# Optimization experiments

Hardware: AMD Instinct MI355X
Metric: run time of the kernel (lower is better)

## Reference

```python
import jax, jax.numpy as jnp
import numpy as np

L, D, H, F, E, K = 2, 512, 8, 2048, 8, 2
V, B, S, T, PAD = 32000, 2, 1024, 1024, 0


def _pe(n, d):
    pos = jnp.arange(n, dtype=jnp.float32)[:, None]
    div = jnp.exp(jnp.arange(0, d, 2, dtype=jnp.float32) * (-np.log(10000.0) / d))
    pe = jnp.zeros((n, d), jnp.float32)
    pe = pe.at[:, 0::2].set(jnp.sin(pos * div)).at[:, 1::2].set(jnp.cos(pos * div))
    return pe


def _ln(x, g, b):
    m = x.mean(-1, keepdims=True)
    v = ((x - m) ** 2).mean(-1, keepdims=True)
    return (x - m) / jnp.sqrt(v + 1e-5) * g + b


def _mha(q_in, k_in, v_in, w, b, mask):
    # w: [4,D,D] (q,k,v,out), b: [4,D]; mask broadcastable to [B,H,Sq,Sk] (True=keep)
    Bq, Sq, Dm = q_in.shape
    Sk = k_in.shape[1]
    dk = Dm // H
    q = (q_in @ w[0] + b[0]).reshape(Bq, Sq, H, dk).transpose(0, 2, 1, 3)
    k = (k_in @ w[1] + b[1]).reshape(Bq, Sk, H, dk).transpose(0, 2, 1, 3)
    v = (v_in @ w[2] + b[2]).reshape(Bq, Sk, H, dk).transpose(0, 2, 1, 3)
    s = jnp.einsum('bhqd,bhkd->bhqk', q, k) / np.sqrt(dk).astype(np.float32)
    s = jnp.where(mask, s, jnp.float32(-1e9))
    a = jax.nn.softmax(s, axis=-1)
    c = jnp.einsum('bhqk,bhkd->bhqd', a, v).transpose(0, 2, 1, 3).reshape(Bq, Sq, Dm)
    return c @ w[3] + b[3]


def _moe(x, gw, gb, w1, b1, w2, b2):
    # token-choice top-k routing with softmax gate probs (no renormalization)
    Bx, Sx, Dm = x.shape
    N = Bx * Sx
    xf = x.reshape(N, Dm)
    probs = jax.nn.softmax(xf @ gw + gb, axis=-1)              # [N,E]
    topv, topi = jax.lax.top_k(probs, K)                        # [N,K]
    comb = jnp.zeros_like(probs).at[jnp.arange(N)[:, None], topi].set(topv)  # [N,E] sparse combine weights
    h = jax.nn.relu(jnp.einsum('nd,edf->nef', xf, w1) + b1)     # [N,E,F]
    eo = jnp.einsum('nef,efd->ned', h, w2) + b2                 # [N,E,D]
    y = jnp.einsum('ne,ned->nd', comb, eo)
    return y.reshape(Bx, Sx, Dm)


def setup_inputs():
    key = jax.random.key(0)
    ks = iter(jax.random.split(key, 32))
    sd, sf = 1.0 / np.sqrt(D), 1.0 / np.sqrt(F)

    def nrm(shape, scale):
        return jax.random.normal(next(ks), shape, jnp.float32) * np.float32(scale)

    inp = {}
    inp['src'] = jax.random.randint(next(ks), (B, S), 0, V)
    inp['tgt'] = jax.random.randint(next(ks), (B, T), 0, V)
    inp['enc_emb'] = nrm((V, D), 0.02).at[PAD].set(0.0)
    inp['dec_emb'] = nrm((V, D), 0.02).at[PAD].set(0.0)
    inp['enc_attn_w'] = nrm((L, 4, D, D), sd)
    inp['enc_attn_b'] = jnp.zeros((L, 4, D), jnp.float32)
    inp['enc_ln_g'] = jnp.ones((L, 2, D), jnp.float32)
    inp['enc_ln_b'] = jnp.zeros((L, 2, D), jnp.float32)
    inp['enc_gate_w'] = nrm((L, D, E), sd)
    inp['enc_gate_b'] = jnp.zeros((L, E), jnp.float32)
    inp['enc_w1'] = nrm((L, E, D, F), sd)
    inp['enc_b1'] = jnp.zeros((L, E, F), jnp.float32)
    inp['enc_w2'] = nrm((L, E, F, D), sf)
    inp['enc_b2'] = jnp.zeros((L, E, D), jnp.float32)
    inp['dec_sa_w'] = nrm((L, 4, D, D), sd)
    inp['dec_sa_b'] = jnp.zeros((L, 4, D), jnp.float32)
    inp['dec_ca_w'] = nrm((L, 4, D, D), sd)
    inp['dec_ca_b'] = jnp.zeros((L, 4, D), jnp.float32)
    inp['dec_ln_g'] = jnp.ones((L, 3, D), jnp.float32)
    inp['dec_ln_b'] = jnp.zeros((L, 3, D), jnp.float32)
    inp['dec_gate_w'] = nrm((L, D, E), sd)
    inp['dec_gate_b'] = jnp.zeros((L, E), jnp.float32)
    inp['dec_w1'] = nrm((L, E, D, F), sd)
    inp['dec_b1'] = jnp.zeros((L, E, F), jnp.float32)
    inp['dec_w2'] = nrm((L, E, F, D), sf)
    inp['dec_b2'] = jnp.zeros((L, E, D), jnp.float32)
    inp['out_w'] = nrm((D, V), sd)
    inp['out_b'] = jnp.zeros((V,), jnp.float32)
    return inp


def reference(src, tgt, enc_emb, dec_emb, enc_attn_w, enc_attn_b, enc_ln_g, enc_ln_b,
              enc_gate_w, enc_gate_b, enc_w1, enc_b1, enc_w2, enc_b2,
              dec_sa_w, dec_sa_b, dec_ca_w, dec_ca_b, dec_ln_g, dec_ln_b,
              dec_gate_w, dec_gate_b, dec_w1, dec_b1, dec_w2, dec_b2, out_w, out_b):
    src_mask = (src != PAD)[:, None, None, :]                                  # [B,1,1,S]
    causal = jnp.tril(jnp.ones((T, T), bool))
    tgt_mask = (tgt != PAD)[:, None, None, :] & causal[None, None]             # [B,1,T,T]

    x = enc_emb[src] + _pe(S, D)[None]                                         # dropout = identity (eval)
    for l in range(L):
        a = _mha(x, x, x, enc_attn_w[l], enc_attn_b[l], src_mask)
        x = _ln(x + a, enc_ln_g[l, 0], enc_ln_b[l, 0])
        f = _moe(x, enc_gate_w[l], enc_gate_b[l], enc_w1[l], enc_b1[l], enc_w2[l], enc_b2[l])
        x = _ln(x + f, enc_ln_g[l, 1], enc_ln_b[l, 1])
    enc_out = x

    y = dec_emb[tgt] + _pe(T, D)[None]
    for l in range(L):
        a = _mha(y, y, y, dec_sa_w[l], dec_sa_b[l], tgt_mask)
        y = _ln(y + a, dec_ln_g[l, 0], dec_ln_b[l, 0])
        c = _mha(y, enc_out, enc_out, dec_ca_w[l], dec_ca_b[l], src_mask)
        y = _ln(y + c, dec_ln_g[l, 1], dec_ln_b[l, 1])
        f = _moe(y, dec_gate_w[l], dec_gate_b[l], dec_w1[l], dec_b1[l], dec_w2[l], dec_b2[l])
        y = _ln(y + f, dec_ln_g[l, 2], dec_ln_b[l, 2])

    return y @ out_w + out_b                                                    # [B,T,V]
```

## Files before the change

### kernel.cpp

```cpp
#include <hip/hip_runtime.h>
#include <hip/hip_bf16.h>

#define L_ 2
#define D_ 512
#define H_ 8
#define DK_ 64
#define F_ 2048
#define E_ 8
#define V_ 32000
#define B_ 2
#define S_ 1024
#define T_ 1024
#define NTOK (B_*S_)
#define MAXPAD 4608
#define RB64   72
#define QLD 1536

typedef unsigned short u16;
typedef _Float16 f16x8 __attribute__((ext_vector_type(8)));
typedef _Float16 f16x4 __attribute__((ext_vector_type(4)));
typedef float f32x4 __attribute__((ext_vector_type(4)));

__device__ __forceinline__ void gload16(const void* g, const void* l) {
    __builtin_amdgcn_global_load_lds(
        (const __attribute__((address_space(1))) void*)g,
        (__attribute__((address_space(3))) void*)l, 16, 0, 0);
}

__device__ __forceinline__ void split_f16(float v, _Float16& h, _Float16& l) {
    h = (_Float16)v;
    l = (_Float16)(v - (float)h);
}

__global__ __launch_bounds__(256) void embed_pe(const int* __restrict__ toks,
                                                const float* __restrict__ emb,
                                                _Float16* __restrict__ oh,
                                                _Float16* __restrict__ ol, int Slen)
{
    int n = blockIdx.x;
    int spos = n % Slen;
    int tok = toks[n];
    const float* erow = emb + (size_t)tok * D_;
    size_t rb = (size_t)n * D_;
    for (int j = threadIdx.x; j < D_; j += 256) {
        int i = j >> 1;
        float arg = (float)spos * expf(-(float)i * 0.035977892f);
        float pe = (j & 1) ? cosf(arg) : sinf(arg);
        float v = erow[j] + pe;
        _Float16 h, l; split_f16(v, h, l);
        oh[rb + j] = h; ol[rb + j] = l;
    }
}

template<bool WLO>
__global__ __launch_bounds__(256) void transpose_w(const float* __restrict__ in,
                                                   _Float16* __restrict__ oh,
                                                   _Float16* __restrict__ ol, int R, int C)
{
    __shared__ float t[64][65];
    size_t sb = (size_t)blockIdx.z * R * C;
    in += sb; oh += sb; if (WLO) ol += sb;
    int c0 = blockIdx.x * 64, r0 = blockIdx.y * 64;
    int tid = threadIdx.x;
    {
        int r = tid >> 4;
        int cq = (tid & 15) * 4;
        #pragma unroll
        for (int p = 0; p < 4; ++p) {
            int rr = r + p * 16;
            float4 v = *(const float4*)&in[(size_t)(r0 + rr) * C + c0 + cq];
            t[rr][cq] = v.x; t[rr][cq + 1] = v.y; t[rr][cq + 2] = v.z; t[rr][cq + 3] = v.w;
        }
    }
    __syncthreads();
    int rp = (tid & 15) * 4;
    int cb = tid >> 4;
    #pragma unroll
    for (int p = 0; p < 4; ++p) {
        int c = cb + p * 16;
        f16x4 hv, lv;
        #pragma unroll
        for (int j = 0; j < 4; ++j) {
            float v = t[rp + j][c];
            _Float16 h = (_Float16)v;
            hv[j] = h;
            if (WLO) lv[j] = (_Float16)(v - (float)h);
        }
        *(f16x4*)&oh[(size_t)(c0 + c) * R + r0 + rp] = hv;
        if (WLO) *(f16x4*)&ol[(size_t)(c0 + c) * R + r0 + rp] = lv;
    }
}

__global__ __launch_bounds__(256) void transpose_w3(
    const float* __restrict__ i0, _Float16* __restrict__ h0, _Float16* __restrict__ l0,
    const float* __restrict__ i1, _Float16* __restrict__ h1, _Float16* __restrict__ l1,
    const float* __restrict__ i2, _Float16* __restrict__ h2, _Float16* __restrict__ l2)
{
    __shared__ float t[64][65];
    int set = blockIdx.z >> 3, sub = blockIdx.z & 7;
    const float* in = (set == 0) ? i0 : (set == 1) ? i1 : i2;
    _Float16* oh = (set == 0) ? h0 : (set == 1) ? h1 : h2;
    _Float16* ol = (set == 0) ? l0 : (set == 1) ? l1 : l2;
    size_t sb = (size_t)sub * D_ * D_;
    in += sb; oh += sb; ol += sb;
    int c0 = blockIdx.x * 64, r0 = blockIdx.y * 64;
    int tid = threadIdx.x;
    {
        int r = tid >> 4;
        int cq = (tid & 15) * 4;
        #pragma unroll
        for (int p = 0; p < 4; ++p) {
            int rr = r + p * 16;
            float4 v = *(const float4*)&in[(size_t)(r0 + rr) * D_ + c0 + cq];
            t[rr][cq] = v.x; t[rr][cq + 1] = v.y; t[rr][cq + 2] = v.z; t[rr][cq + 3] = v.w;
        }
    }
    __syncthreads();
    int rp = (tid & 15) * 4;
    int cb = tid >> 4;
    #pragma unroll
    for (int p = 0; p < 4; ++p) {
        int c = cb + p * 16;
        f16x4 hv, lv;
        #pragma unroll
        for (int j = 0; j < 4; ++j) {
            float v = t[rp + j][c];
            _Float16 h = (_Float16)v;
            hv[j] = h;
            lv[j] = (_Float16)(v - (float)h);
        }
        *(f16x4*)&oh[(size_t)(c0 + c) * D_ + r0 + rp] = hv;
        *(f16x4*)&ol[(size_t)(c0 + c) * D_ + r0 + rp] = lv;
    }
}

template<int MODE, bool RELU, int OUTMODE, int PASSES, int TM, int TN>
__global__ __launch_bounds__(256, 2) void gemm_mfma(
    const _Float16* __restrict__ Ah, const _Float16* __restrict__ Al,
    const _Float16* __restrict__ Wh, const _Float16* __restrict__ Wl,
    const float* __restrict__ biasbase,
    float* __restrict__ Cf, _Float16* __restrict__ Ch, _Float16* __restrict__ Cl,
    _Float16* __restrict__ vt_h, _Float16* __restrict__ vt_l, int cbase,
    int M, int Kd, int N, int ldc,
    const int* __restrict__ route_tok, const int* __restrict__ rb_expert,
    const int* __restrict__ pad_base, const int* __restrict__ counts)
{
    constexpr int AR = TM / 32;
    constexpr int BR = TN / 32;
    int row0 = blockIdx.x * TM;
    const _Float16* Wmh = Wh;
    const _Float16* Wml = Wl;
    const float* bias = biasbase;
    int vend = M;
    if (MODE != 0) {
        int total = pad_base[E_];
        if (row0 >= total) return;
        int e = rb_expert[row0 >> 6];
        vend = pad_base[e] + counts[e];
        Wmh = Wh + (size_t)e * Kd * N;
        if (PASSES == 3) Wml = Wl + (size_t)e * Kd * N;
        bias = biasbase + (size_t)e * N;
    }
    int col0 = blockIdx.y * TN;
    int tid = threadIdx.x;
    int lane = tid & 63, w = tid >> 6;
    int wm = w >> 1, wn = w & 1;

    __shared__ _Float16 lds[(PASSES == 3 ? 2 : 1) * (TM + TN) * 64];
    _Float16* lAh = lds;
    _Float16* lBh = lds + TM * 64;
    _Float16* lAl = (PASSES == 3) ? lds + (TM + TN) * 64 : nullptr;
    _Float16* lBl = (PASSES == 3) ? lds + (TM + TN) * 64 + TM * 64 : nullptr;

    int srow8 = lane >> 3;
    int q8 = lane & 7;
    size_t aoff[AR], boff[BR];
    #pragma unroll
    for (int j = 0; j < AR; ++j) {
        int m = w * (TM / 4) + j * 8 + srow8;
        int gr = row0 + m;
        int ar = (MODE == 1) ? route_tok[gr] : gr;
        int ss = (q8 ^ (m & 7)) << 3;
        aoff[j] = (size_t)ar * Kd + ss;
    }
    #pragma unroll
    for (int j = 0; j < BR; ++j) {
        int m = w * (TN / 4) + j * 8 + srow8;
        int ss = (q8 ^ (m & 7)) << 3;
        boff[j] = (size_t)(col0 + m) * Kd + ss;
    }

    f32x4 zero4 = {0.f, 0.f, 0.f, 0.f};
    f32x4 acc[AR][BR];
    #pragma unroll
    for (int i = 0; i < AR; ++i)
        #pragma unroll
        for (int j = 0; j < BR; ++j) acc[i][j] = zero4;

    int lm = lane & 15, kg = lane >> 4;

    for (int k0 = 0; k0 < Kd; k0 += 64) {
        #pragma unroll
        for (int j = 0; j < AR; ++j) {
            int lb = (w * (TM / 4) + j * 8) * 64;
            gload16(Ah + aoff[j] + k0, lAh + lb);
            if (PASSES == 3) gload16(Al + aoff[j] + k0, lAl + lb);
        }
        #pragma unroll
        for (int j = 0; j < BR; ++j) {
            int lb = (w * (TN / 4) + j * 8) * 64;
            gload16(Wmh + boff[j] + k0, lBh + lb);
            if (PASSES == 3) gload16(Wml + boff[j] + k0, lBl + lb);
        }
        __syncthreads();
        #pragma unroll
        for (int ks = 0; ks < 2; ++ks) {
            f16x8 ah[AR], bh[BR];
            #pragma unroll
            for (int i = 0; i < AR; ++i) {
                int m = wm * (TM / 2) + i * 16 + lm;
                ah[i] = *(const f16x8*)&lAh[m * 64 + ((((ks << 2) + kg) ^ (m & 7)) << 3)];
            }
            #pragma unroll
            for (int j = 0; j < BR; ++j) {
                int n = wn * (TN / 2) + j * 16 + lm;
                bh[j] = *(const f16x8*)&lBh[n * 64 + ((((ks << 2) + kg) ^ (n & 7)) << 3)];
            }
            #pragma unroll
            for (int i = 0; i < AR; ++i)
                #pragma unroll
                for (int jn = 0; jn < BR; ++jn)
                    acc[i][jn] = __builtin_amdgcn_mfma_f32_16x16x32_f16(ah[i], bh[jn], acc[i][jn], 0, 0, 0);
            if (PASSES == 3) {
                f16x8 bl[BR];
                #pragma unroll
                for (int j = 0; j < BR; ++j) {
                    int n = wn * (TN / 2) + j * 16 + lm;
                    bl[j] = *(const f16x8*)&lBl[n * 64 + ((((ks << 2) + kg) ^ (n & 7)) << 3)];
                }
                #pragma unroll
                for (int i = 0; i < AR; ++i)
                    #pragma unroll
                    for (int jn = 0; jn < BR; ++jn)
                        acc[i][jn] = __builtin_amdgcn_mfma_f32_16x16x32_f16(ah[i], bl[jn], acc[i][jn], 0, 0, 0);
                f16x8 al[AR];
                #pragma unroll
                for (int i = 0; i < AR; ++i) {
                    int m = wm * (TM / 2) + i * 16 + lm;
                    al[i] = *(const f16x8*)&lAl[m * 64 + ((((ks << 2) + kg) ^ (m & 7)) << 3)];
                }
                #pragma unroll
                for (int i = 0; i < AR; ++i)
                    #pragma unroll
                    for (int jn = 0; jn < BR; ++jn)
                        acc[i][jn] = __builtin_amdgcn_mfma_f32_16x16x32_f16(al[i], bh[jn], acc[i][jn], 0, 0, 0);
            }
        }
        __syncthreads();
    }

    float bv[BR];
    #pragma unroll
    for (int jn = 0; jn < BR; ++jn) bv[jn] = bias[col0 + wn * (TN / 2) + jn * 16 + lm];
    int rowb = row0 + wm * (TM / 2) + (lane >> 4) * 4;

    if (OUTMODE == 2 && (col0 + cbase) >= 1024) {
        #pragma unroll
        for (int i = 0; i < AR; ++i) {
            int row = rowb + i * 16;
            int b = row >> 10, q = row & 1023;
            #pragma unroll
            for (int jn = 0; jn < BR; ++jn) {
                int vcol = col0 + cbase - 1024 + wn * (TN / 2) + jn * 16 + lm;
                int hh = vcol >> 6, dd = vcol & 63;
                f16x4 hv, lv;
                #pragma unroll
                for (int r = 0; r < 4; ++r) {
                    float v = acc[i][jn][r] + bv[jn];
                    _Float16 x1, x2; split_f16(v, x1, x2);
                    hv[r] = x1; lv[r] = x2;
                }
                size_t vtoff = ((size_t)((b << 3) + hh) * 64 + dd) * 1024 + q;
                *(f16x4*)&vt_h[vtoff] = hv;
                *(f16x4*)&vt_l[vtoff] = lv;
            }
        }
        return;
    }

    #pragma unroll
    for (int i = 0; i < AR; ++i) {
        #pragma unroll
        for (int r = 0; r < 4; ++r) {
            int row = rowb + i * 16 + r;
            if (MODE != 0 && row >= vend) continue;
            #pragma unroll
            for (int jn = 0; jn < BR; ++jn) {
                float v = acc[i][jn][r] + bv[jn];
                if (RELU) v = fmaxf(v, 0.f);
                int c = col0 + wn * (TN / 2) + jn * 16 + lm;
                if (OUTMODE == 0) {
                    Cf[(size_t)row * ldc + c] = v;
                } else {
                    _Float16 h, l; split_f16(v, h, l);
                    Ch[(size_t)row * ldc + cbase + c] = h;
                    Cl[(size_t)row * ldc + cbase + c] = l;
                }
            }
        }
    }
}

template<int CAUSAL>
__global__ __launch_bounds__(512, 1) void attn_flash(
    const _Float16* __restrict__ qkvh, const _Float16* __restrict__ qkvl,
    const _Float16* __restrict__ vth, const _Float16* __restrict__ vtl,
    const int* __restrict__ ktoks,
    _Float16* __restrict__ ch, _Float16* __restrict__ cl)
{
    int q0 = blockIdx.x * 64;
    int bh = blockIdx.y, b = bh >> 3, h = bh & 7;
    int tid = threadIdx.x, lane = tid & 63, w = tid >> 6;
    int qg = w & 3, kh = w >> 2;
    int lm = lane & 15, kg = lane >> 4;
    int srow8 = lane >> 3, q8 = lane & 7;
    int tb = b * S_;

    __shared__ _Float16 smem[49152];
    _Float16* hb  = smem + kh * 16384;
    _Float16* lKh = hb;
    _Float16* lKl = hb + 4096;
    _Float16* lVh = hb + 8192;
    _Float16* lVl = hb + 12288;
    _Float16* lPh = smem + 32768 + w * 1024;
    _Float16* lPl = smem + 40960 + w * 1024;

    size_t qbase = (size_t)b * S_ * QLD + h * DK_;
    const _Float16* Qh = qkvh + qbase;
    const _Float16* Ql = qkvl + qbase;
    const _Float16* Kh = qkvh + qbase + 512;
    const _Float16* Kl = qkvl + qbase + 512;
    const _Float16* Vh = vth + (size_t)bh * 64 * 1024;
    const _Float16* Vl = vtl + (size_t)bh * 64 * 1024;

    f16x8 qfh[2], qfl[2];
    {
        int qr = q0 + qg * 16 + lm;
        #pragma unroll
        for (int ks = 0; ks < 2; ++ks) {
            qfh[ks] = *(const f16x8*)&Qh[(size_t)qr * QLD + ks * 32 + kg * 8];
            qfl[ks] = *(const f16x8*)&Ql[(size_t)qr * QLD + ks * 32 + kg * 8];
        }
    }

    float mreg[4], lreg[4];
    f32x4 od[4];
    f32x4 zero4 = {0.f, 0.f, 0.f, 0.f};
    #pragma unroll
    for (int r = 0; r < 4; ++r) { mreg[r] = -1e30f; lreg[r] = 0.f; }
    #pragma unroll
    for (int jn = 0; jn < 4; ++jn) od[jn] = zero4;

    int qrow[4];
    #pragma unroll
    for (int r = 0; r < 4; ++r) qrow[r] = q0 + qg * 16 + (lane >> 4) * 4 + r;

    int nkt = CAUSAL ? (q0 >> 6) + 1 : 16;
    int nhalf = (nkt + 1) >> 1;

    for (int it = 0; it < nhalf; ++it) {
        int kt = 2 * it + kh;
        bool active = kt < nkt;
        int k0 = kt * 64;

        if (active) {
            #pragma unroll
            for (int j = 0; j < 2; ++j) {
                int row = qg * 16 + j * 8 + srow8;
                int lb = (qg * 16 + j * 8) * 64;
                int ss = (q8 ^ (row & 7)) << 3;
                gload16(Kh + (size_t)(k0 + row) * QLD + ss, lKh + lb);
                gload16(Kl + (size_t)(k0 + row) * QLD + ss, lKl + lb);
                gload16(Vh + (size_t)row * 1024 + k0 + ss, lVh + lb);
                gload16(Vl + (size_t)row * 1024 + k0 + ss, lVl + lb);
            }
        }
        __syncthreads();

        if (active) {
            bool diag = CAUSAL && (kt == (q0 >> 6));
            f32x4 accs[4];
            #pragma unroll
            for (int jn = 0; jn < 4; ++jn) accs[jn] = zero4;
            #pragma unroll
            for (int ks = 0; ks < 2; ++ks) {
                #pragma unroll
                for (int jn = 0; jn < 4; ++jn) {
                    int n = jn * 16 + lm;
                    int koff = n * 64 + ((((ks << 2) + kg) ^ (n & 7)) << 3);
                    f16x8 bhv = *(const f16x8*)&lKh[koff];
                    f16x8 blv = *(const f16x8*)&lKl[koff];
                    accs[jn] = __builtin_amdgcn_mfma_f32_16x16x32_f16(qfh[ks], bhv, accs[jn], 0, 0, 0);
                    accs[jn] = __builtin_amdgcn_mfma_f32_16x16x32_f16(qfh[ks], blv, accs[jn], 0, 0, 0);
                    accs[jn] = __builtin_amdgcn_mfma_f32_16x16x32_f16(qfl[ks], bhv, accs[jn], 0, 0, 0);
                }
            }

            float sv[4][4];
            #pragma unroll
            for (int jn = 0; jn < 4; ++jn) {
                int kglob = k0 + jn * 16 + lm;
                bool pad_ok = (ktoks[tb + kglob] != 0);
                #pragma unroll
                for (int r = 0; r < 4; ++r) {
                    float s = accs[jn][r] * 0.125f;
                    bool keep = pad_ok && (!diag || kglob <= qrow[r]);
                    sv[jn][r] = keep ? s : -1e9f;
                }
            }
            float pv[4][4];
            #pragma unroll
            for (int r = 0; r < 4; ++r) {
                float tm = fmaxf(fmaxf(sv[0][r], sv[1][r]), fmaxf(sv[2][r], sv[3][r]));
                tm = fmaxf(tm, __shfl_xor(tm, 1));
                tm = fmaxf(tm, __shfl_xor(tm, 2));
                tm = fmaxf(tm, __shfl_xor(tm, 4));
                tm = fmaxf(tm, __shfl_xor(tm, 8));
                float mnew = fmaxf(mreg[r], tm);
                float corr = expf(mreg[r] - mnew);
                lreg[r] *= corr;
                #pragma unroll
                for (int jn = 0; jn < 4; ++jn) od[jn][r] *= corr;
                float psum = 0.f;
                #pragma unroll
                for (int jn = 0; jn < 4; ++jn) {
                    float p = expf(sv[jn][r] - mnew);
                    pv[jn][r] = p;
                    psum += p;
                }
                psum += __shfl_xor(psum, 1);
                psum += __shfl_xor(psum, 2);
                psum += __shfl_xor(psum, 4);
                psum += __shfl_xor(psum, 8);
                lreg[r] += psum;
                mreg[r] = mnew;
            }

            #pragma unroll
            for (int jn = 0; jn < 4; ++jn) {
                int col = jn * 16 + lm;
                #pragma unroll
                for (int r = 0; r < 4; ++r) {
                    int rr = (lane >> 4) * 4 + r;
                    int idx = rr * 64 + (((col >> 3) ^ (rr & 7)) << 3) + (col & 7);
                    _Float16 hh, ll; split_f16(pv[jn][r], hh, ll);
                    lPh[idx] = hh; lPl[idx] = ll;
                }
            }

            #pragma unroll
            for (int ks = 0; ks < 2; ++ks) {
                int poff = lm * 64 + ((((ks << 2) + kg) ^ (lm & 7)) << 3);
                f16x8 pah = *(const f16x8*)&lPh[poff];
                f16x8 pal = *(const f16x8*)&lPl[poff];
                #pragma unroll
                for (int jn = 0; jn < 4; ++jn) {
                    int n = jn * 16 + lm;
                    int noff = n * 64 + ((((ks << 2) + kg) ^ (n & 7)) << 3);
                    f16x8 vbh = *(const f16x8*)&lVh[noff];
                    f16x8 vbl = *(const f16x8*)&lVl[noff];
                    od[jn] = __builtin_amdgcn_mfma_f32_16x16x32_f16(pah, vbh, od[jn], 0, 0, 0);
                    od[jn] = __builtin_amdgcn_mfma_f32_16x16x32_f16(pah, vbl, od[jn], 0, 0, 0);
                    od[jn] = __builtin_amdgcn_mfma_f32_16x16x32_f16(pal, vbh, od[jn], 0, 0, 0);
                }
            }
        }
        __syncthreads();
    }

    float* mrg = (float*)(smem + 32768);
    if (kh == 1) {
        float* mp = mrg + ((size_t)qg * 64 + lane) * 24;
        #pragma unroll
        for (int jn = 0; jn < 4; ++jn)
            #pragma unroll
            for (int r = 0; r < 4; ++r) mp[jn * 4 + r] = od[jn][r];
        #pragma unroll
        for (int r = 0; r < 4; ++r) { mp[16 + r] = mreg[r]; mp[20 + r] = lreg[r]; }
    }
    __syncthreads();
    if (kh == 0) {
        float* mp = mrg + ((size_t)qg * 64 + lane) * 24;
        #pragma unroll
        for (int r = 0; r < 4; ++r) {
            float m1 = mp[16 + r], l1 = mp[20 + r];
            float m = fmaxf(mreg[r], m1);
            float c0 = expf(mreg[r] - m), c1 = expf(m1 - m);
            float inv = 1.0f / (lreg[r] * c0 + l1 * c1);
            size_t rbase = (size_t)(tb + qrow[r]) * D_ + h * DK_;
            #pragma unroll
            for (int jn = 0; jn < 4; ++jn) {
                float o = (od[jn][r] * c0 + mp[jn * 4 + r] * c1) * inv;
                _Float16 hh, ll; split_f16(o, hh, ll);
                int d = jn * 16 + lm;
                ch[rbase + d] = hh; cl[rbase + d] = ll;
            }
        }
    }
}

template<bool GATE>
__global__ __launch_bounds__(256) void ln_add(const _Float16* __restrict__ xh,
                                              const _Float16* __restrict__ xl,
                                              const float* __restrict__ r,
                                              const float* __restrict__ g,
                                              const float* __restrict__ be,
                                              _Float16* __restrict__ oh,
                                              _Float16* __restrict__ ol,
                                              const float* __restrict__ gw,
                                              const float* __restrict__ gbias,
                                              float* __restrict__ lg)
{
    int w = threadIdx.x >> 6, lane = threadIdx.x & 63;
    int row = blockIdx.x * 4 + w;
    int col = lane * 8;
    size_t rb = (size_t)row * D_ + col;
    f16x8 vh = *(const f16x8*)&xh[rb];
    f16x8 vl = *(const f16x8*)&xl[rb];
    float4 ra = *(const float4*)&r[rb];
    float4 rc = *(const float4*)&r[rb + 4];
    float v[8];
    v[0] = (float)vh[0] + (float)vl[0] + ra.x;
    v[1] = (float)vh[1] + (float)vl[1] + ra.y;
    v[2] = (float)vh[2] + (float)vl[2] + ra.z;
    v[3] = (float)vh[3] + (float)vl[3] + ra.w;
    v[4] = (float)vh[4] + (float)vl[4] + rc.x;
    v[5] = (float)vh[5] + (float)vl[5] + rc.y;
    v[6] = (float)vh[6] + (float)vl[6] + rc.z;
    v[7] = (float)vh[7] + (float)vl[7] + rc.w;
    float s = 0.f;
    #pragma unroll
    for (int i = 0; i < 8; ++i) s += v[i];
    #pragma unroll
    for (int off = 32; off; off >>= 1) s += __shfl_xor(s, off);
    float m = s * (1.0f / 512.0f);
    float d[8];
    float q = 0.f;
    #pragma unroll
    for (int i = 0; i < 8; ++i) { d[i] = v[i] - m; q += d[i] * d[i]; }
    #pragma unroll
    for (int off = 32; off; off >>= 1) q += __shfl_xor(q, off);
    float rstd = rsqrtf(q * (1.0f / 512.0f) + 1e-5f);
    float4 ga = *(const float4*)&g[col];
    float4 gc = *(const float4*)&g[col + 4];
    float4 ba = *(const float4*)&be[col];
    float4 bc = *(const float4*)&be[col + 4];
    float gg[8] = {ga.x, ga.y, ga.z, ga.w, gc.x, gc.y, gc.z, gc.w};
    float bb[8] = {ba.x, ba.y, ba.z, ba.w, bc.x, bc.y, bc.z, bc.w};
    float y[8];
    f16x8 ohv, olv;
    #pragma unroll
    for (int i = 0; i < 8; ++i) {
        y[i] = d[i] * rstd * gg[i] + bb[i];
        _Float16 h2, l2; split_f16(y[i], h2, l2);
        ohv[i] = h2; olv[i] = l2;
    }
    *(f16x8*)&oh[rb] = ohv;
    *(f16x8*)&ol[rb] = olv;
    if (GATE) {
        float acc[E_] = {0.f, 0.f, 0.f, 0.f, 0.f, 0.f, 0.f, 0.f};
        #pragma unroll
        for (int i = 0; i < 8; ++i) {
            const float* gp = gw + (size_t)(col + i) * E_;
            float4 g0 = *(const float4*)gp;
            float4 g1 = *(const float4*)(gp + 4);
            acc[0] += y[i] * g0.x; acc[1] += y[i] * g0.y;
            acc[2] += y[i] * g0.z; acc[3] += y[i] * g0.w;
            acc[4] += y[i] * g1.x; acc[5] += y[i] * g1.y;
            acc[6] += y[i] * g1.z; acc[7] += y[i] * g1.w;
        }
        #pragma unroll
        for (int e = 0; e < E_; ++e)
            #pragma unroll
            for (int off = 32; off; off >>= 1) acc[e] += __shfl_xor(acc[e], off);
        if (lane == 0) {
            float* lp = lg + (size_t)row * E_;
            #pragma unroll
            for (int e = 0; e < E_; ++e) lp[e] = acc[e] + gbias[e];
        }
    }
}

__global__ __launch_bounds__(256) void ln_add_moe(const _Float16* __restrict__ xh,
                                                  const _Float16* __restrict__ xl,
                                                  const float* __restrict__ eo,
                                                  const float* __restrict__ topv,
                                                  const int* __restrict__ route_row,
                                                  const float* __restrict__ g,
                                                  const float* __restrict__ be,
                                                  _Float16* __restrict__ oh,
                                                  _Float16* __restrict__ ol)
{
    int w = threadIdx.x >> 6, lane = threadIdx.x & 63;
    int row = blockIdx.x * 4 + w;
    int r0 = route_row[row * 2], r1 = route_row[row * 2 + 1];
    float w0 = topv[row * 2], w1 = topv[row * 2 + 1];
    int col = lane * 8;
    size_t rb = (size_t)row * D_ + col;
    f16x8 vh = *(const f16x8*)&xh[rb];
    f16x8 vl = *(const f16x8*)&xl[rb];
    const float* e0 = eo + (size_t)r0 * D_ + col;
    const float* e1 = eo + (size_t)r1 * D_ + col;
    float4 e0a = *(const float4*)e0;
    float4 e0b = *(const float4*)(e0 + 4);
    float4 e1a = *(const float4*)e1;
    float4 e1b = *(const float4*)(e1 + 4);
    float v[8];
    v[0] = (float)vh[0] + (float)vl[0] + w0 * e0a.x + w1 * e1a.x;
    v[1] = (float)vh[1] + (float)vl[1] + w0 * e0a.y + w1 * e1a.y;
    v[2] = (float)vh[2] + (float)vl[2] + w0 * e0a.z + w1 * e1a.z;
    v[3] = (float)vh[3] + (float)vl[3] + w0 * e0a.w + w1 * e1a.w;
    v[4] = (float)vh[4] + (float)vl[4] + w0 * e0b.x + w1 * e1b.x;
    v[5] = (float)vh[5] + (float)vl[5] + w0 * e0b.y + w1 * e1b.y;
    v[6] = (float)vh[6] + (float)vl[6] + w0 * e0b.z + w1 * e1b.z;
    v[7] = (float)vh[7] + (float)vl[7] + w0 * e0b.w + w1 * e1b.w;
    float s = 0.f;
    #pragma unroll
    for (int i = 0; i < 8; ++i) s += v[i];
    #pragma unroll
    for (int off = 32; off; off >>= 1) s += __shfl_xor(s, off);
    float m = s * (1.0f / 512.0f);
    float d[8];
    float q = 0.f;
// ... 85 lines not shown
        for (int sg = 0; sg < 16; ++sg) {
            int v = segb[t][sg];
            segb[t][sg] = (unsigned short)run;
            run += v;
        }
        cnt[t] = run;
        counts[t] = run;
    }
    __syncthreads();
    if (t < 128) {
        int e = t >> 4, seg = t & 15;
        int run = segb[e][seg];
        #pragma unroll
        for (int i = 0; i < 16; ++i) {
            int c = seg * 16 + i;
            int v = chist[c][e];
            chist[c][e] = (unsigned short)run;
            run += v;
        }
    }
    __syncthreads();

    if (t == 0) {
        int pad = 0;
        for (int e = 0; e < 8; ++e) {
            pb[e] = pad;
            pad_base[e] = pad;
            int nb = (cnt[e] + 63) >> 6;
            for (int rb = 0; rb < nb; ++rb) rb_expert[(pad >> 6) + rb] = e;
            pad += nb << 6;
        }
        pb[8] = pad;
        pad_base[8] = pad;
    }
    __syncthreads();

    if (t < 256) {
        int r[16];
        #pragma unroll
        for (int i = 0; i < 16; ++i) r[i] = eid[t * 16 + i];
        #pragma unroll
        for (int e = 0; e < 8; ++e) {
            int o = pb[e] + chist[t][e];
            #pragma unroll
            for (int i = 0; i < 16; ++i) {
                if (r[i] == e) {
                    int slot = t * 16 + i;
                    route_tok[o] = slot >> 1;
                    route_row[slot] = o;
                    o++;
                }
            }
        }
    }
}

extern "C" void kernel_launch(void* const* d_in, const int* in_sizes, int n_in,
                              void* d_out, int out_size, void* d_ws, size_t ws_size,
                              hipStream_t stream)
{
    const int*   src        = (const int*)  d_in[0];
    const int*   tgt        = (const int*)  d_in[1];
    const float* enc_emb    = (const float*)d_in[2];
    const float* dec_emb    = (const float*)d_in[3];
    const float* enc_attn_w = (const float*)d_in[4];
    const float* enc_attn_b = (const float*)d_in[5];
    const float* enc_ln_g   = (const float*)d_in[6];
    const float* enc_ln_b   = (const float*)d_in[7];
    const float* enc_gate_w = (const float*)d_in[8];
    const float* enc_gate_b = (const float*)d_in[9];
    const float* enc_w1     = (const float*)d_in[10];
    const float* enc_b1     = (const float*)d_in[11];
    const float* enc_w2     = (const float*)d_in[12];
    const float* enc_b2     = (const float*)d_in[13];
    const float* dec_sa_w   = (const float*)d_in[14];
    const float* dec_sa_b   = (const float*)d_in[15];
    const float* dec_ca_w   = (const float*)d_in[16];
    const float* dec_ca_b   = (const float*)d_in[17];
    const float* dec_ln_g   = (const float*)d_in[18];
    const float* dec_ln_b   = (const float*)d_in[19];
    const float* dec_gate_w = (const float*)d_in[20];
    const float* dec_gate_b = (const float*)d_in[21];
    const float* dec_w1     = (const float*)d_in[22];
    const float* dec_b1     = (const float*)d_in[23];
    const float* dec_w2     = (const float*)d_in[24];
    const float* dec_b2     = (const float*)d_in[25];
    const float* out_w      = (const float*)d_in[26];
    const float* out_b      = (const float*)d_in[27];
    float* out = (float*)d_out;

    char* ob = (char*)d_out;
    size_t oc = 0;
    auto dalloc = [&](size_t bytes) { char* p = ob + oc; oc += (bytes + 255) & ~(size_t)255; return p; };
    _Float16* qkv_h  = (_Float16*)dalloc((size_t)NTOK * QLD * 2);
    _Float16* qkv_l  = (_Float16*)dalloc((size_t)NTOK * QLD * 2);
    _Float16* vt_h   = (_Float16*)dalloc((size_t)16 * 64 * 1024 * 2);
    _Float16* vt_l   = (_Float16*)dalloc((size_t)16 * 64 * 1024 * 2);
    float* aout  = (float*)dalloc((size_t)NTOK * D_ * 4);
    _Float16* ctx_h = (_Float16*)dalloc((size_t)NTOK * D_ * 2);
    _Float16* ctx_l = (_Float16*)dalloc((size_t)NTOK * D_ * 2);
    _Float16* encA_h = (_Float16*)dalloc((size_t)L_ * 4 * D_ * D_ * 2);
    _Float16* encA_l = (_Float16*)dalloc((size_t)L_ * 4 * D_ * D_ * 2);
    _Float16* saA_h  = (_Float16*)dalloc((size_t)L_ * 4 * D_ * D_ * 2);
    _Float16* saA_l  = (_Float16*)dalloc((size_t)L_ * 4 * D_ * D_ * 2);
    _Float16* caA_h  = (_Float16*)dalloc((size_t)L_ * 4 * D_ * D_ * 2);
    _Float16* caA_l  = (_Float16*)dalloc((size_t)L_ * 4 * D_ * D_ * 2);
    _Float16* xA_h = (_Float16*)dalloc((size_t)NTOK * D_ * 2);
    _Float16* xA_l = (_Float16*)dalloc((size_t)NTOK * D_ * 2);
    _Float16* xB_h = (_Float16*)dalloc((size_t)NTOK * D_ * 2);
    _Float16* xB_l = (_Float16*)dalloc((size_t)NTOK * D_ * 2);
    _Float16* yA_h = (_Float16*)dalloc((size_t)NTOK * D_ * 2);
    _Float16* yA_l = (_Float16*)dalloc((size_t)NTOK * D_ * 2);
    _Float16* yB_h = (_Float16*)dalloc((size_t)NTOK * D_ * 2);
    _Float16* yB_l = (_Float16*)dalloc((size_t)NTOK * D_ * 2);

    char* wp = (char*)d_ws;
    size_t wc = 0;
    auto walloc = [&](size_t bytes) { char* p = wp + wc; wc += (bytes + 255) & ~(size_t)255; return p; };
    _Float16* outwT_h = (_Float16*)walloc((size_t)V_ * D_ * 2);
    _Float16* final_h = (_Float16*)walloc((size_t)NTOK * D_ * 2);
    size_t wsz = (size_t)L_ * E_ * D_ * F_;
    _Float16* ew1t_h = (_Float16*)walloc(wsz * 2);
    _Float16* ew1t_l = (_Float16*)walloc(wsz * 2);
    _Float16* ew2t_h = (_Float16*)walloc(wsz * 2);
    _Float16* ew2t_l = (_Float16*)walloc(wsz * 2);
    _Float16* dw1t_h = (_Float16*)walloc(wsz * 2);
    _Float16* dw1t_l = (_Float16*)walloc(wsz * 2);
    _Float16* dw2t_h = (_Float16*)walloc(wsz * 2);
    _Float16* dw2t_l = (_Float16*)walloc(wsz * 2);
    _Float16* hbuf_h  = (_Float16*)walloc((size_t)5120 * F_ * 2);
    _Float16* hbuf_l  = (_Float16*)walloc((size_t)5120 * F_ * 2);
    float*    eobuf   = (float*)walloc((size_t)5120 * D_ * 4);
    float* lg   = (float*)walloc((size_t)NTOK * E_ * 4);
    float* topv = (float*)walloc((size_t)NTOK * 2 * 4);
    int*   route_tok = (int*)walloc((size_t)5120 * 4);
    int*   route_row = (int*)walloc((size_t)NTOK * 2 * 4);
    int*   counts    = (int*)walloc(64);
    int*   pad_base  = (int*)walloc(64);
    int*   rb_expert = (int*)walloc((size_t)128 * 4);

    transpose_w3<<<dim3(8, 8, 24), 256, 0, stream>>>(
        enc_attn_w, encA_h, encA_l, dec_sa_w, saA_h, saA_l, dec_ca_w, caA_h, caA_l);
    transpose_w<false><<<dim3(500, 8, 1), 256, 0, stream>>>(out_w, outwT_h, nullptr, D_, V_);
    transpose_w<true><<<dim3(32, 8, L_ * E_), 256, 0, stream>>>(enc_w1, ew1t_h, ew1t_l, D_, F_);
    transpose_w<true><<<dim3(8, 32, L_ * E_), 256, 0, stream>>>(enc_w2, ew2t_h, ew2t_l, F_, D_);
    transpose_w<true><<<dim3(32, 8, L_ * E_), 256, 0, stream>>>(dec_w1, dw1t_h, dw1t_l, D_, F_);
    transpose_w<true><<<dim3(8, 32, L_ * E_), 256, 0, stream>>>(dec_w2, dw2t_h, dw2t_l, F_, D_);

    auto run_mha = [&](const _Float16* q_h, const _Float16* q_l,
                       const _Float16* kv_h, const _Float16* kv_l,
                       const _Float16* wT_h, const _Float16* wT_l, const float* bt,
                       const int* ktoks, int causal, bool fused) {
        if (fused) {
            gemm_mfma<0, false, 2, 3, 64, 128><<<dim3(32, 12), 256, 0, stream>>>(
                q_h, q_l, wT_h, wT_l, bt, nullptr, qkv_h, qkv_l, vt_h, vt_l, 0,
                NTOK, D_, 1536, QLD, nullptr, nullptr, nullptr, nullptr);
        } else {
            gemm_mfma<0, false, 1, 3, 64, 64><<<dim3(32, 8), 256, 0, stream>>>(
                q_h, q_l, wT_h, wT_l, bt, nullptr, qkv_h, qkv_l, nullptr, nullptr, 0,
                NTOK, D_, 512, QLD, nullptr, nullptr, nullptr, nullptr);
            gemm_mfma<0, false, 2, 3, 64, 128><<<dim3(32, 8), 256, 0, stream>>>(
                kv_h, kv_l, wT_h + (size_t)D_ * D_, wT_l + (size_t)D_ * D_, bt + D_,
                nullptr, qkv_h, qkv_l, vt_h, vt_l, 512,
                NTOK, D_, 1024, QLD, nullptr, nullptr, nullptr, nullptr);
        }
        if (causal)
            attn_flash<1><<<dim3(16, 16), 512, 0, stream>>>(qkv_h, qkv_l, vt_h, vt_l, ktoks, ctx_h, ctx_l);
        else
            attn_flash<0><<<dim3(16, 16), 512, 0, stream>>>(qkv_h, qkv_l, vt_h, vt_l, ktoks, ctx_h, ctx_l);
        gemm_mfma<0, false, 0, 3, 64, 64><<<dim3(32, 8), 256, 0, stream>>>(
            ctx_h, ctx_l, wT_h + (size_t)3 * D_ * D_, wT_l + (size_t)3 * D_ * D_,
            bt + 3 * D_, aout, nullptr, nullptr, nullptr, nullptr, 0,
            NTOK, D_, 512, 512, nullptr, nullptr, nullptr, nullptr);
    };

    auto run_moe = [&](const _Float16* x_h, const _Float16* x_l,
                       const _Float16* w1h, const _Float16* w1l,
                       const _Float16* w2h, const _Float16* w2l,
                       const float* b1p, const float* b2p, bool p3) {
        gate_top2_routes<<<1, 1024, 0, stream>>>(lg, topv, route_tok, route_row, counts, pad_base, rb_expert);
        if (p3) {
            gemm_mfma<1, true, 1, 3, 64, 128><<<dim3(RB64, 16), 256, 0, stream>>>(
                x_h, x_l, w1h, w1l, b1p, nullptr, hbuf_h, hbuf_l, nullptr, nullptr, 0,
                0, D_, F_, F_, route_tok, rb_expert, pad_base, counts);
            gemm_mfma<2, false, 0, 3, 64, 64><<<dim3(RB64, 8), 256, 0, stream>>>(
                hbuf_h, hbuf_l, w2h, w2l, b2p, eobuf, nullptr, nullptr, nullptr, nullptr, 0,
                0, F_, D_, D_, route_tok, rb_expert, pad_base, counts);
        } else {
            gemm_mfma<1, true, 1, 1, 64, 128><<<dim3(RB64, 16), 256, 0, stream>>>(
                x_h, nullptr, w1h, nullptr, b1p, nullptr, hbuf_h, hbuf_l, nullptr, nullptr, 0,
                0, D_, F_, F_, route_tok, rb_expert, pad_base, counts);
            gemm_mfma<2, false, 0, 1, 64, 64><<<dim3(RB64, 8), 256, 0, stream>>>(
                hbuf_h, nullptr, w2h, nullptr, b2p, eobuf, nullptr, nullptr, nullptr, nullptr, 0,
                0, F_, D_, D_, route_tok, rb_expert, pad_base, counts);
        }
    };

    embed_pe<<<B_ * S_, 256, 0, stream>>>(src, enc_emb, xA_h, xA_l, S_);
    _Float16* cur_h = xA_h; _Float16* cur_l = xA_l;
    _Float16* alt_h = xB_h; _Float16* alt_l = xB_l;
    for (int l = 0; l < L_; ++l) {
        run_mha(cur_h, cur_l, nullptr, nullptr,
                encA_h + (size_t)l * 4 * D_ * D_, encA_l + (size_t)l * 4 * D_ * D_,
                enc_attn_b + (size_t)l * 4 * D_, src, 0, true);
        ln_add<true><<<NTOK / 4, 256, 0, stream>>>(cur_h, cur_l, aout,
            enc_ln_g + (size_t)(l * 2 + 0) * D_, enc_ln_b + (size_t)(l * 2 + 0) * D_,
            alt_h, alt_l, enc_gate_w + (size_t)l * D_ * E_, enc_gate_b + (size_t)l * E_, lg);
        { _Float16* t = cur_h; cur_h = alt_h; alt_h = t; t = cur_l; cur_l = alt_l; alt_l = t; }
        run_moe(cur_h, cur_l,
                ew1t_h + (size_t)l * E_ * D_ * F_, ew1t_l + (size_t)l * E_ * D_ * F_,
                ew2t_h + (size_t)l * E_ * D_ * F_, ew2t_l + (size_t)l * E_ * D_ * F_,
                enc_b1 + (size_t)l * E_ * F_, enc_b2 + (size_t)l * E_ * D_, true);
        ln_add_moe<<<NTOK / 4, 256, 0, stream>>>(cur_h, cur_l, eobuf, topv, route_row,
            enc_ln_g + (size_t)(l * 2 + 1) * D_, enc_ln_b + (size_t)(l * 2 + 1) * D_,
            alt_h, alt_l);
        { _Float16* t = cur_h; cur_h = alt_h; alt_h = t; t = cur_l; cur_l = alt_l; alt_l = t; }
    }
    _Float16* enc_h = cur_h; _Float16* enc_l = cur_l;

    embed_pe<<<B_ * T_, 256, 0, stream>>>(tgt, dec_emb, yA_h, yA_l, T_);
    _Float16* dc_h = yA_h; _Float16* dc_l = yA_l;
    _Float16* da_h = yB_h; _Float16* da_l = yB_l;
    for (int l = 0; l < L_; ++l) {
        run_mha(dc_h, dc_l, nullptr, nullptr,
                saA_h + (size_t)l * 4 * D_ * D_, saA_l + (size_t)l * 4 * D_ * D_,
                dec_sa_b + (size_t)l * 4 * D_, tgt, 1, true);
        ln_add<false><<<NTOK / 4, 256, 0, stream>>>(dc_h, dc_l, aout,
            dec_ln_g + (size_t)(l * 3 + 0) * D_, dec_ln_b + (size_t)(l * 3 + 0) * D_,
            da_h, da_l, nullptr, nullptr, nullptr);
        { _Float16* t = dc_h; dc_h = da_h; da_h = t; t = dc_l; dc_l = da_l; da_l = t; }
        run_mha(dc_h, dc_l, enc_h, enc_l,
                caA_h + (size_t)l * 4 * D_ * D_, caA_l + (size_t)l * 4 * D_ * D_,
                dec_ca_b + (size_t)l * 4 * D_, src, 0, false);
        ln_add<true><<<NTOK / 4, 256, 0, stream>>>(dc_h, dc_l, aout,
            dec_ln_g + (size_t)(l * 3 + 1) * D_, dec_ln_b + (size_t)(l * 3 + 1) * D_,
            da_h, da_l, dec_gate_w + (size_t)l * D_ * E_, dec_gate_b + (size_t)l * E_, lg);
        { _Float16* t = dc_h; dc_h = da_h; da_h = t; t = dc_l; dc_l = da_l; da_l = t; }
        bool last = (l == L_ - 1);
        run_moe(dc_h, dc_l,
                dw1t_h + (size_t)l * E_ * D_ * F_, dw1t_l + (size_t)l * E_ * D_ * F_,
                dw2t_h + (size_t)l * E_ * D_ * F_, dw2t_l + (size_t)l * E_ * D_ * F_,
                dec_b1 + (size_t)l * E_ * F_, dec_b2 + (size_t)l * E_ * D_, !last);
        ln_add_moe<<<NTOK / 4, 256, 0, stream>>>(dc_h, dc_l, eobuf, topv, route_row,
            dec_ln_g + (size_t)(l * 3 + 2) * D_, dec_ln_b + (size_t)(l * 3 + 2) * D_,
            last ? final_h : da_h, da_l);
        { _Float16* t = dc_h; dc_h = da_h; da_h = t; t = dc_l; dc_l = da_l; da_l = t; }
    }

    gemm_mfma<0, false, 0, 1, 128, 128><<<dim3(NTOK / 128, V_ / 128), 256, 0, stream>>>(
        final_h, nullptr, outwT_h, nullptr, out_b, out, nullptr, nullptr, nullptr, nullptr, 0,
        NTOK, D_, V_, V_, nullptr, nullptr, nullptr, nullptr);
}
```

Measured before the change: 1.199 ms.

## Use eight waves per GEMM block with a 2x4 wave layout

Doubles each GEMM block from 256 to 512 threads and rearranges the waves from a 2x2 to a 2x4 grid, so each wave computes half as many output columns. Global-to-LDS copy duties are spread over the eight waves, and every launch site now uses 512 threads. The aim is more waves to hide memory latency and shorter per-wave MFMA chains. In exchange, each A fragment is read from LDS by more waves, and the new launch bounds of (512, 4) tighten the register budget, which could cause spills in the 128x128 and three-pass variants.

```diff
diff --git a/kernel.cpp b/kernel.cpp
--- a/kernel.cpp
+++ b/kernel.cpp
@@ -135,7 +135,7 @@
 }
 
 template<int MODE, bool RELU, int OUTMODE, int PASSES, int TM, int TN>
-__global__ __launch_bounds__(256, 2) void gemm_mfma(
+__global__ __launch_bounds__(512, 4) void gemm_mfma(
     const _Float16* __restrict__ Ah, const _Float16* __restrict__ Al,
     const _Float16* __restrict__ Wh, const _Float16* __restrict__ Wl,
     const float* __restrict__ biasbase,
@@ -145,8 +145,10 @@
     const int* __restrict__ route_tok, const int* __restrict__ rb_expert,
     const int* __restrict__ pad_base, const int* __restrict__ counts)
 {
-    constexpr int AR = TM / 32;
-    constexpr int BR = TN / 32;
+    constexpr int ARW = TM / 32;
+    constexpr int BRW = TN / 64;
+    constexpr int AISS = TM / 64;
+    constexpr int BISS = TN / 64;
     int row0 = blockIdx.x * TM;
     const _Float16* Wmh = Wh;
     const _Float16* Wml = Wl;
@@ -164,7 +166,7 @@
     int col0 = blockIdx.y * TN;
     int tid = threadIdx.x;
     int lane = tid & 63, w = tid >> 6;
-    int wm = w >> 1, wn = w & 1;
+    int wm = w >> 2, wn = w & 3;
 
     __shared__ _Float16 lds[(PASSES == 3 ? 2 : 1) * (TM + TN) * 64];
     _Float16* lAh = lds;
@@ -174,104 +176,104 @@
 
     int srow8 = lane >> 3;
     int q8 = lane & 7;
-    size_t aoff[AR], boff[BR];
-    #pragma unroll
-    for (int j = 0; j < AR; ++j) {
-        int m = w * (TM / 4) + j * 8 + srow8;
+    size_t aoff[AISS], boff[BISS];
+    #pragma unroll
+    for (int j = 0; j < AISS; ++j) {
+        int m = w * (TM / 8) + j * 8 + srow8;
         int gr = row0 + m;
         int ar = (MODE == 1) ? route_tok[gr] : gr;
         int ss = (q8 ^ (m & 7)) << 3;
         aoff[j] = (size_t)ar * Kd + ss;
     }
     #pragma unroll
-    for (int j = 0; j < BR; ++j) {
-        int m = w * (TN / 4) + j * 8 + srow8;
+    for (int j = 0; j < BISS; ++j) {
+        int m = w * (TN / 8) + j * 8 + srow8;
         int ss = (q8 ^ (m & 7)) << 3;
         boff[j] = (size_t)(col0 + m) * Kd + ss;
     }
 
     f32x4 zero4 = {0.f, 0.f, 0.f, 0.f};
-    f32x4 acc[AR][BR];
-    #pragma unroll
-    for (int i = 0; i < AR; ++i)
-        #pragma unroll
-        for (int j = 0; j < BR; ++j) acc[i][j] = zero4;
+    f32x4 acc[ARW][BRW];
+    #pragma unroll
+    for (int i = 0; i < ARW; ++i)
+        #pragma unroll
+        for (int j = 0; j < BRW; ++j) acc[i][j] = zero4;
 
     int lm = lane & 15, kg = lane >> 4;
 
     for (int k0 = 0; k0 < Kd; k0 += 64) {
         #pragma unroll
-        for (int j = 0; j < AR; ++j) {
-            int lb = (w * (TM / 4) + j * 8) * 64;
+        for (int j = 0; j < AISS; ++j) {
+            int lb = (w * (TM / 8) + j * 8) * 64;
             gload16(Ah + aoff[j] + k0, lAh + lb);
             if (PASSES == 3) gload16(Al + aoff[j] + k0, lAl + lb);
         }
         #pragma unroll
-        for (int j = 0; j < BR; ++j) {
-            int lb = (w * (TN / 4) + j * 8) * 64;
+        for (int j = 0; j < BISS; ++j) {
+            int lb = (w * (TN / 8) + j * 8) * 64;
             gload16(Wmh + boff[j] + k0, lBh + lb);
             if (PASSES == 3) gload16(Wml + boff[j] + k0, lBl + lb);
         }
         __syncthreads();
         #pragma unroll
         for (int ks = 0; ks < 2; ++ks) {
-            f16x8 ah[AR], bh[BR];
-            #pragma unroll
-            for (int i = 0; i < AR; ++i) {
+            f16x8 ah[ARW], bh[BRW];
+            #pragma unroll
+            for (int i = 0; i < ARW; ++i) {
                 int m = wm * (TM / 2) + i * 16 + lm;
                 ah[i] = *(const f16x8*)&lAh[m * 64 + ((((ks << 2) + kg) ^ (m & 7)) << 3)];
             }
             #pragma unroll
-            for (int j = 0; j < BR; ++j) {
-                int n = wn * (TN / 2) + j * 16 + lm;
+            for (int j = 0; j < BRW; ++j) {
+                int n = wn * (TN / 4) + j * 16 + lm;
                 bh[j] = *(const f16x8*)&lBh[n * 64 + ((((ks << 2) + kg) ^ (n & 7)) << 3)];
             }
             #pragma unroll
-            for (int i = 0; i < AR; ++i)
-                #pragma unroll
-                for (int jn = 0; jn < BR; ++jn)
+            for (int i = 0; i < ARW; ++i)
+                #pragma unroll
+                for (int jn = 0; jn < BRW; ++jn)
                     acc[i][jn] = __builtin_amdgcn_mfma_f32_16x16x32_f16(ah[i], bh[jn], acc[i][jn], 0, 0, 0);
             if (PASSES == 3) {
-                f16x8 bl[BR];
-                #pragma unroll
-                for (int j = 0; j < BR; ++j) {
-                    int n = wn * (TN / 2) + j * 16 + lm;
+                f16x8 bl[BRW];
+                #pragma unroll
+                for (int j = 0; j < BRW; ++j) {
+                    int n = wn * (TN / 4) + j * 16 + lm;
                     bl[j] = *(const f16x8*)&lBl[n * 64 + ((((ks << 2) + kg) ^ (n & 7)) << 3)];
                 }
                 #pragma unroll
-                for (int i = 0; i < AR; ++i)
+                for (int i = 0; i < ARW; ++i)
                     #pragma unroll
-                    for (int jn = 0; jn < BR; ++jn)
+                    for (int jn = 0; jn < BRW; ++jn)
                         acc[i][jn] = __builtin_amdgcn_mfma_f32_16x16x32_f16(ah[i], bl[jn], acc[i][jn], 0, 0, 0);
-                f16x8 al[AR];
-                #pragma unroll
-                for (int i = 0; i < AR; ++i) {
+                f16x8 al[ARW];
+                #pragma unroll
+                for (int i = 0; i < ARW; ++i) {
                     int m = wm * (TM / 2) + i * 16 + lm;
                     al[i] = *(const f16x8*)&lAl[m * 64 + ((((ks << 2) + kg) ^ (m & 7)) << 3)];
                 }
                 #pragma unroll
-                for (int i = 0; i < AR; ++i)
+                for (int i = 0; i < ARW; ++i)
                     #pragma unroll
-                    for (int jn = 0; jn < BR; ++jn)
+                    for (int jn = 0; jn < BRW; ++jn)
                         acc[i][jn] = __builtin_amdgcn_mfma_f32_16x16x32_f16(al[i], bh[jn], acc[i][jn], 0, 0, 0);
             }
         }
         __syncthreads();
     }
 
-    float bv[BR];
-    #pragma unroll
-    for (int jn = 0; jn < BR; ++jn) bv[jn] = bias[col0 + wn * (TN / 2) + jn * 16 + lm];
+    float bv[BRW];
+    #pragma unroll
+    for (int jn = 0; jn < BRW; ++jn) bv[jn] = bias[col0 + wn * (TN / 4) + jn * 16 + lm];
     int rowb = row0 + wm * (TM / 2) + (lane >> 4) * 4;
 
     if (OUTMODE == 2 && (col0 + cbase) >= 1024) {
         #pragma unroll
-        for (int i = 0; i < AR; ++i) {
+        for (int i = 0; i < ARW; ++i) {
             int row = rowb + i * 16;
             int b = row >> 10, q = row & 1023;
             #pragma unroll
-            for (int jn = 0; jn < BR; ++jn) {
-                int vcol = col0 + cbase - 1024 + wn * (TN / 2) + jn * 16 + lm;
+            for (int jn = 0; jn < BRW; ++jn) {
+                int vcol = col0 + cbase - 1024 + wn * (TN / 4) + jn * 16 + lm;
                 int hh = vcol >> 6, dd = vcol & 63;
                 f16x4 hv, lv;
                 #pragma unroll
@@ -289,16 +291,16 @@
     }
 
     #pragma unroll
-    for (int i = 0; i < AR; ++i) {
+    for (int i = 0; i < ARW; ++i) {
         #pragma unroll
         for (int r = 0; r < 4; ++r) {
             int row = rowb + i * 16 + r;
             if (MODE != 0 && row >= vend) continue;
             #pragma unroll
-            for (int jn = 0; jn < BR; ++jn) {
+            for (int jn = 0; jn < BRW; ++jn) {
                 float v = acc[i][jn][r] + bv[jn];
                 if (RELU) v = fmaxf(v, 0.f);
-                int c = col0 + wn * (TN / 2) + jn * 16 + lm;
+                int c = col0 + wn * (TN / 4) + jn * 16 + lm;
                 if (OUTMODE == 0) {
                     Cf[(size_t)row * ldc + c] = v;
                 } else {
@@ -870,14 +872,14 @@
                        const _Float16* wT_h, const _Float16* wT_l, const float* bt,
                        const int* ktoks, int causal, bool fused) {
         if (fused) {
-            gemm_mfma<0, false, 2, 3, 64, 128><<<dim3(32, 12), 256, 0, stream>>>(
+            gemm_mfma<0, false, 2, 3, 64, 128><<<dim3(32, 12), 512, 0, stream>>>(
                 q_h, q_l, wT_h, wT_l, bt, nullptr, qkv_h, qkv_l, vt_h, vt_l, 0,
                 NTOK, D_, 1536, QLD, nullptr, nullptr, nullptr, nullptr);
         } else {
-            gemm_mfma<0, false, 1, 3, 64, 64><<<dim3(32, 8), 256, 0, stream>>>(
+            gemm_mfma<0, false, 1, 3, 64, 64><<<dim3(32, 8), 512, 0, stream>>>(
                 q_h, q_l, wT_h, wT_l, bt, nullptr, qkv_h, qkv_l, nullptr, nullptr, 0,
                 NTOK, D_, 512, QLD, nullptr, nullptr, nullptr, nullptr);
-            gemm_mfma<0, false, 2, 3, 64, 128><<<dim3(32, 8), 256, 0, stream>>>(
+            gemm_mfma<0, false, 2, 3, 64, 128><<<dim3(32, 8), 512, 0, stream>>>(
                 kv_h, kv_l, wT_h + (size_t)D_ * D_, wT_l + (size_t)D_ * D_, bt + D_,
                 nullptr, qkv_h, qkv_l, vt_h, vt_l, 512,
                 NTOK, D_, 1024, QLD, nullptr, nullptr, nullptr, nullptr);
@@ -886,7 +888,7 @@
             attn_flash<1><<<dim3(16, 16), 512, 0, stream>>>(qkv_h, qkv_l, vt_h, vt_l, ktoks, ctx_h, ctx_l);
         else
             attn_flash<0><<<dim3(16, 16), 512, 0, stream>>>(qkv_h, qkv_l, vt_h, vt_l, ktoks, ctx_h, ctx_l);
-        gemm_mfma<0, false, 0, 3, 64, 64><<<dim3(32, 8), 256, 0, stream>>>(
+        gemm_mfma<0, false, 0, 3, 64, 64><<<dim3(32, 8), 512, 0, stream>>>(
             ctx_h, ctx_l, wT_h + (size_t)3 * D_ * D_, wT_l + (size_t)3 * D_ * D_,
             bt + 3 * D_, aout, nullptr, nullptr, nullptr, nullptr, 0,
             NTOK, D_, 512, 512, nullptr, nullptr, nullptr, nullptr);
@@ -898,17 +900,17 @@
                        const float* b1p, const float* b2p, bool p3) {
         gate_top2_routes<<<1, 1024, 0, stream>>>(lg, topv, route_tok, route_row, counts, pad_base, rb_expert);
         if (p3) {
-            gemm_mfma<1, true, 1, 3, 64, 128><<<dim3(RB64, 16), 256, 0, stream>>>(
+            gemm_mfma<1, true, 1, 3, 64, 128><<<dim3(RB64, 16), 512, 0, stream>>>(
                 x_h, x_l, w1h, w1l, b1p, nullptr, hbuf_h, hbuf_l, nullptr, nullptr, 0,
                 0, D_, F_, F_, route_tok, rb_expert, pad_base, counts);
-            gemm_mfma<2, false, 0, 3, 64, 64><<<dim3(RB64, 8), 256, 0, stream>>>(
+            gemm_mfma<2, false, 0, 3, 64, 64><<<dim3(RB64, 8), 512, 0, stream>>>(
                 hbuf_h, hbuf_l, w2h, w2l, b2p, eobuf, nullptr, nullptr, nullptr, nullptr, 0,
                 0, F_, D_, D_, route_tok, rb_expert, pad_base, counts);
         } else {
-            gemm_mfma<1, true, 1, 1, 64, 128><<<dim3(RB64, 16), 256, 0, stream>>>(
+            gemm_mfma<1, true, 1, 1, 64, 128><<<dim3(RB64, 16), 512, 0, stream>>>(
                 x_h, nullptr, w1h, nullptr, b1p, nullptr, hbuf_h, hbuf_l, nullptr, nullptr, 0,
                 0, D_, F_, F_, route_tok, rb_expert, pad_base, counts);
-            gemm_mfma<2, false, 0, 1, 64, 64><<<dim3(RB64, 8), 256, 0, stream>>>(
+            gemm_mfma<2, false, 0, 1, 64, 64><<<dim3(RB64, 8), 512, 0, stream>>>(
                 hbuf_h, nullptr, w2h, nullptr, b2p, eobuf, nullptr, nullptr, nullptr, nullptr, 0,
                 0, F_, D_, D_, route_tok, rb_expert, pad_base, counts);
         }
@@ -965,7 +967,7 @@
         { _Float16* t = dc_h; dc_h = da_h; da_h = t; t = dc_l; dc_l = da_l; da_l = t; }
     }
 
-    gemm_mfma<0, false, 0, 1, 128, 128><<<dim3(NTOK / 128, V_ / 128), 256, 0, stream>>>(
+    gemm_mfma<0, false, 0, 1, 128, 128><<<dim3(NTOK / 128, V_ / 128), 512, 0, stream>>>(
         final_h, nullptr, outwT_h, nullptr, out_b, out, nullptr, nullptr, nullptr, nullptr, 0,
         NTOK, D_, V_, V_, nullptr, nullptr, nullptr, nullptr);
 }
```

Measured after the change: 1.213 ms. About the same (+1.2%).

## Share one P buffer for hi/lo halves to cut LDS and raise occupancy

Applied to the files above, without the earlier changes.

The attention kernel no longer keeps separate LDS buffers for the high and low f16 halves of the softmax probabilities. It writes the high half, runs its MFMAs, then overwrites the same buffer with the residual low half and runs the remaining MFMAs. This cuts shared memory from 96KB to 80KB so two blocks could share a CU. The launch bound is raised to 4 blocks per CU. The cost is more LDS writes, a second pass of V-tile reads, and a tight register budget that may force spills.

```diff
diff --git a/kernel.cpp b/kernel.cpp
--- a/kernel.cpp
+++ b/kernel.cpp
@@ -312,7 +312,7 @@
 }
 
 template<int CAUSAL>
-__global__ __launch_bounds__(512, 1) void attn_flash(
+__global__ __launch_bounds__(512, 4) void attn_flash(
     const _Float16* __restrict__ qkvh, const _Float16* __restrict__ qkvl,
     const _Float16* __restrict__ vth, const _Float16* __restrict__ vtl,
     const int* __restrict__ ktoks,
@@ -326,14 +326,13 @@
     int srow8 = lane >> 3, q8 = lane & 7;
     int tb = b * S_;
 
-    __shared__ _Float16 smem[49152];
+    __shared__ _Float16 smem[40960];
     _Float16* hb  = smem + kh * 16384;
     _Float16* lKh = hb;
     _Float16* lKl = hb + 4096;
     _Float16* lVh = hb + 8192;
     _Float16* lVl = hb + 12288;
-    _Float16* lPh = smem + 32768 + w * 1024;
-    _Float16* lPl = smem + 40960 + w * 1024;
+    _Float16* lP  = smem + 32768 + w * 1024;
 
     size_t qbase = (size_t)b * S_ * QLD + h * DK_;
     const _Float16* Qh = qkvh + qbase;
@@ -453,16 +452,13 @@
                 for (int r = 0; r < 4; ++r) {
                     int rr = (lane >> 4) * 4 + r;
                     int idx = rr * 64 + (((col >> 3) ^ (rr & 7)) << 3) + (col & 7);
-                    _Float16 hh, ll; split_f16(pv[jn][r], hh, ll);
-                    lPh[idx] = hh; lPl[idx] = ll;
-                }
-            }
-
+                    lP[idx] = (_Float16)pv[jn][r];
+                }
+            }
             #pragma unroll
             for (int ks = 0; ks < 2; ++ks) {
                 int poff = lm * 64 + ((((ks << 2) + kg) ^ (lm & 7)) << 3);
-                f16x8 pah = *(const f16x8*)&lPh[poff];
-                f16x8 pal = *(const f16x8*)&lPl[poff];
+                f16x8 pah = *(const f16x8*)&lP[poff];
                 #pragma unroll
                 for (int jn = 0; jn < 4; ++jn) {
                     int n = jn * 16 + lm;
@@ -471,6 +467,28 @@
                     f16x8 vbl = *(const f16x8*)&lVl[noff];
                     od[jn] = __builtin_amdgcn_mfma_f32_16x16x32_f16(pah, vbh, od[jn], 0, 0, 0);
                     od[jn] = __builtin_amdgcn_mfma_f32_16x16x32_f16(pah, vbl, od[jn], 0, 0, 0);
+                }
+            }
+            #pragma unroll
+            for (int jn = 0; jn < 4; ++jn) {
+                int col = jn * 16 + lm;
+                #pragma unroll
+                for (int r = 0; r < 4; ++r) {
+                    int rr = (lane >> 4) * 4 + r;
+                    int idx = rr * 64 + (((col >> 3) ^ (rr & 7)) << 3) + (col & 7);
+                    float p = pv[jn][r];
+                    lP[idx] = (_Float16)(p - (float)(_Float16)p);
+                }
+            }
+            #pragma unroll
+            for (int ks = 0; ks < 2; ++ks) {
+                int poff = lm * 64 + ((((ks << 2) + kg) ^ (lm & 7)) << 3);
+                f16x8 pal = *(const f16x8*)&lP[poff];
+                #pragma unroll
+                for (int jn = 0; jn < 4; ++jn) {
+                    int n = jn * 16 + lm;
+                    int noff = n * 64 + ((((ks << 2) + kg) ^ (n & 7)) << 3);
+                    f16x8 vbh = *(const f16x8*)&lVh[noff];
                     od[jn] = __builtin_amdgcn_mfma_f32_16x16x32_f16(pal, vbh, od[jn], 0, 0, 0);
                 }
             }
@@ -478,7 +496,7 @@
         __syncthreads();
     }
 
-    float* mrg = (float*)(smem + 32768);
+    float* mrg = (float*)smem;
     if (kh == 1) {
         float* mp = mrg + ((size_t)qg * 64 + lane) * 24;
         #pragma unroll
```

New measurement: 1.282 ms. +6.9%, slower.
